# Kernel optimization log

Hardware: AMD Instinct MI355X
Metric: run time of the kernel (lower is better)

Reference implementation:

```python
import jax, jax.numpy as jnp
import numpy as np


def setup_inputs() -> dict:
    key = jax.random.key(0)
    k1, k2, k3 = jax.random.split(key, 3)
    B, L, H = 4, 4096, 1024
    x = jax.random.normal(k1, (B, L, H), dtype=jnp.float32)
    # 0.02 scale keeps attention logits in a sane range (like trained weights)
    in_proj_weight = jax.random.normal(k2, (3 * H, H), dtype=jnp.float32) * 0.02
    in_proj_bias = jnp.zeros((3 * H,), dtype=jnp.float32)
    out_proj_weight = jax.random.normal(k3, (H, H), dtype=jnp.float32) * 0.02
    out_proj_bias = jnp.zeros((H,), dtype=jnp.float32)
    return {
        "x": x,
        "in_proj_weight": in_proj_weight,
        "in_proj_bias": in_proj_bias,
        "out_proj_weight": out_proj_weight,
        "out_proj_bias": out_proj_bias,
        "num_heads": 16,
        "window_size": 128,
    }


def _windowed_mha(x, in_proj_weight, in_proj_bias, out_proj_weight, out_proj_bias,
                  num_heads, window_size):
    B, L, H = x.shape
    P = window_size
    pad = (-L) % P  # static
    xp = jnp.pad(x, ((0, 0), (0, pad), (0, 0))) if pad else x
    Lp = xp.shape[1]
    nw = Lp // P
    w = xp.reshape(B * nw, P, H)  # [NW, P, H]
    # packed QKV projection (torch MHA: q,k,v = split(x @ W_in.T + b_in))
    qkv = jnp.einsum('nph,dh->npd', w, in_proj_weight) + in_proj_bias
    q, k, v = jnp.split(qkv, 3, axis=-1)
    hd = H // num_heads

    def to_heads(t):
        return t.reshape(B * nw, P, num_heads, hd).transpose(0, 2, 1, 3)  # [NW, Hh, P, hd]

    q, k, v = to_heads(q), to_heads(k), to_heads(v)
    scale = 1.0 / jnp.sqrt(jnp.asarray(hd, dtype=x.dtype))
    scores = jnp.einsum('nhqd,nhkd->nhqk', q * scale, k)  # [NW, Hh, P, P]
    attn = jax.nn.softmax(scores, axis=-1)
    o = jnp.einsum('nhqk,nhkd->nhqd', attn, v)  # [NW, Hh, P, hd]
    o = o.transpose(0, 2, 1, 3).reshape(B * nw, P, H)
    o = jnp.einsum('nph,oh->npo', o, out_proj_weight) + out_proj_bias
    o = o.reshape(B, Lp, H)
    return o[:, :L]


def reference(x, in_proj_weight, in_proj_bias, out_proj_weight, out_proj_bias,
              num_heads, window_size):
    return _windowed_mha(x, in_proj_weight, in_proj_bias, out_proj_weight,
                         out_proj_bias, num_heads, window_size)
```

## Files before the change

### kernel.cpp

```cpp
#include <hip/hip_runtime.h>
#include <hip/hip_bf16.h>
#include <cstdint>


typedef __bf16 bf16_t;
typedef __bf16 bf16x8 __attribute__((ext_vector_type(8)));
typedef __bf16 bf16x4 __attribute__((ext_vector_type(4)));
typedef float  floatx4 __attribute__((ext_vector_type(4)));

#define MFMA_16x16x32(A, B, C) __builtin_amdgcn_mfma_f32_16x16x32_bf16(A, B, C, 0, 0, 0)

__device__ __forceinline__ void gld_lds16(const bf16_t* g, bf16_t* l) {
  __builtin_amdgcn_global_load_lds(
      (__attribute__((address_space(1))) void*)(void*)(g),
      (__attribute__((address_space(3))) void*)(l), 16, 0, 0);
}

__device__ __forceinline__ void cvt8(const float* __restrict__ s,
                                     bf16_t* __restrict__ d) {
  float4 a = ((const float4*)s)[0];
  float4 b = ((const float4*)s)[1];
  bf16x8 o;
  o[0] = (bf16_t)a.x; o[1] = (bf16_t)a.y; o[2] = (bf16_t)a.z; o[3] = (bf16_t)a.w;
  o[4] = (bf16_t)b.x; o[5] = (bf16_t)b.y; o[6] = (bf16_t)b.z; o[7] = (bf16_t)b.w;
  *(bf16x8*)d = o;
}

__global__ void cvt_all(const float* __restrict__ x,
                        const float* __restrict__ Win,
                        const float* __restrict__ Wout,
                        bf16_t* __restrict__ xb,
                        bf16_t* __restrict__ Wpk,
                        bf16_t* __restrict__ Woutb) {
  const int idx = blockIdx.x * 256 + threadIdx.x;
  if (idx < 2097152) {
    cvt8(x + (size_t)idx * 8, xb + (size_t)idx * 8);
  } else if (idx < 2228224) {
    const int i = idx - 2097152;
    cvt8(Wout + (size_t)i * 8, Woutb + (size_t)i * 8);
  } else {
    const int c = idx - 2228224;
    const int dr = c >> 7, i = c & 127;
    const int head = dr / 192, s = dr - head * 192;
    const int src = (s < 64) ? head * 64 + s
                  : (s < 128) ? 1024 + head * 64 + (s - 64)
                              : 2048 + head * 64 + (s - 128);
    cvt8(Win + (size_t)src * 1024 + i * 8, Wpk + (size_t)dr * 1024 + i * 8);
  }
}

__global__ __launch_bounds__(256, 2) void gemm_out(
    const bf16_t* __restrict__ A, const bf16_t* __restrict__ Bm,
    const float* __restrict__ bias, float* __restrict__ C,
    int M, int N, int K) {
  __shared__ bf16_t As[128 * 64];
  __shared__ bf16_t Bs[256 * 64];
  const int tid  = threadIdx.x;
  const int lane = tid & 63;
  const int wave = tid >> 6;
  const int n16  = lane & 15;
  const int q4   = lane >> 4;
  const int wm   = (wave >> 1) * 64;
  const int wn   = (wave & 1) * 128;
  const int m0   = blockIdx.y * 128;
  const int n0   = blockIdx.x * 256;

  floatx4 acc[4][8] = {};

  for (int k0 = 0; k0 < K; k0 += 64) {
    __syncthreads();
#pragma unroll
    for (int it = 0; it < 4; ++it) {
      const int ch = it * 256 + tid;
      const int r  = ch >> 3;
      const int c8 = (ch & 7) ^ (r & 7);
      gld_lds16(A + (size_t)(m0 + r) * K + k0 + c8 * 8,
                As + (it * 256 + wave * 64) * 8);
    }
#pragma unroll
    for (int it = 0; it < 8; ++it) {
      const int ch = it * 256 + tid;
      const int r  = ch >> 3;
      const int c8 = (ch & 7) ^ (r & 7);
      gld_lds16(Bm + (size_t)(n0 + r) * K + k0 + c8 * 8,
                Bs + (it * 256 + wave * 64) * 8);
    }
    __syncthreads();

#pragma unroll
    for (int half = 0; half < 2; ++half) {
      bf16x8 af[4], bfr[8];
#pragma unroll
      for (int i = 0; i < 4; ++i) {
        const int row = wm + i * 16 + n16;
        af[i] = *(const bf16x8*)&As[row * 64 + (((half * 4 + q4) ^ (row & 7)) * 8)];
      }
#pragma unroll
      for (int j = 0; j < 8; ++j) {
        const int row = wn + j * 16 + n16;
        bfr[j] = *(const bf16x8*)&Bs[row * 64 + (((half * 4 + q4) ^ (row & 7)) * 8)];
      }
#pragma unroll
      for (int i = 0; i < 4; ++i)
#pragma unroll
        for (int j = 0; j < 8; ++j)
          acc[i][j] = MFMA_16x16x32(af[i], bfr[j], acc[i][j]);
    }
  }

#pragma unroll
  for (int i = 0; i < 4; ++i)
#pragma unroll
    for (int j = 0; j < 8; ++j) {
      const int col = n0 + wn + j * 16 + n16;
      const float b = bias[col];
#pragma unroll
      for (int r = 0; r < 4; ++r) {
        const int row = m0 + wm + i * 16 + q4 * 4 + r;
        C[(size_t)row * N + col] = acc[i][j][r] + b;
      }
    }
}

__global__ __launch_bounds__(256, 3) void qkv_attn(
    const bf16_t* __restrict__ X,
    const bf16_t* __restrict__ Wpk,
    const float* __restrict__ bin,
    bf16_t* __restrict__ o)
{
  __shared__ bf16_t smem[26624];
  bf16_t* Xs  = smem;
  bf16_t* Ws  = smem + 8192;
  bf16_t* qs  = smem;
  bf16_t* ks  = smem + 9216;
  bf16_t* vsT = smem + 18432;
  bf16_t* Ps  = smem;

  const int wid  = blockIdx.x;
  const int h    = blockIdx.y;
  const int tid  = threadIdx.x;
  const int lane = tid & 63;
  const int wave = tid >> 6;
  const int n16  = lane & 15;
  const int q4   = lane >> 4;
  const int wm   = (wave >> 1) * 64;
  const int wn   = (wave & 1) * 96;

  const bf16_t* Xg = X + (size_t)wid * 128 * 1024;
  const bf16_t* Wg = Wpk + (size_t)h * 192 * 1024;

  floatx4 acc[4][6] = {};
  for (int k0 = 0; k0 < 1024; k0 += 64) {
    __syncthreads();
#pragma unroll
    for (int it = 0; it < 4; ++it) {
      const int ch = it * 256 + tid;
      const int r  = ch >> 3;
      const int c8 = (ch & 7) ^ (r & 7);
      gld_lds16(Xg + (size_t)r * 1024 + k0 + c8 * 8,
                Xs + (it * 256 + wave * 64) * 8);
    }
#pragma unroll
    for (int it = 0; it < 6; ++it) {
      const int ch = it * 256 + tid;
      const int r  = ch >> 3;
      const int c8 = (ch & 7) ^ (r & 7);
      gld_lds16(Wg + (size_t)r * 1024 + k0 + c8 * 8,
                Ws + (it * 256 + wave * 64) * 8);
    }
    __syncthreads();

#pragma unroll
    for (int half = 0; half < 2; ++half) {
      bf16x8 af[4], bfr[6];
#pragma unroll
      for (int i = 0; i < 4; ++i) {
        const int row = wm + i * 16 + n16;
        af[i] = *(const bf16x8*)&Xs[row * 64 + (((half * 4 + q4) ^ (row & 7)) * 8)];
      }
#pragma unroll
      for (int j = 0; j < 6; ++j) {
        const int row = wn + j * 16 + n16;
        bfr[j] = *(const bf16x8*)&Ws[row * 64 + (((half * 4 + q4) ^ (row & 7)) * 8)];
      }
#pragma unroll
      for (int i = 0; i < 4; ++i)
#pragma unroll
        for (int j = 0; j < 6; ++j)
          acc[i][j] = MFMA_16x16x32(af[i], bfr[j], acc[i][j]);
    }
  }
  __syncthreads();

#pragma unroll
  for (int j = 0; j < 6; ++j) {
    const int base = wn + j * 16;
    const int col  = base + n16;
    const int gb = (base < 64) ? h * 64 + col
                 : (base < 128) ? 1024 + h * 64 + (col - 64)
                                : 2048 + h * 64 + (col - 128);
    const float bias = bin[gb];
#pragma unroll
    for (int i = 0; i < 4; ++i) {
      const int row0 = wm + i * 16 + q4 * 4;
      if (base < 64) {
#pragma unroll
        for (int r = 0; r < 4; ++r)
          qs[(row0 + r) * 72 + col] = (bf16_t)((acc[i][j][r] + bias) * 0.125f);
      } else if (base < 128) {
#pragma unroll
        for (int r = 0; r < 4; ++r)
          ks[(row0 + r) * 72 + (col - 64)] = (bf16_t)(acc[i][j][r] + bias);
      } else {
        bf16x4 pv;
#pragma unroll
        for (int r = 0; r < 4; ++r) pv[r] = (bf16_t)(acc[i][j][r] + bias);
        const int d = col - 128;
        const int c8 = row0 >> 3, pos = row0 & 7;
        *(bf16x4*)&vsT[d * 128 + ((c8 ^ n16) << 3) + pos] = pv;
      }
    }
  }
  __syncthreads();

  floatx4 sacc[2][8] = {};
#pragma unroll
  for (int ks0 = 0; ks0 < 2; ++ks0) {
    bf16x8 aq[2];
#pragma unroll
    for (int i = 0; i < 2; ++i)
      aq[i] = *(const bf16x8*)&qs[(wave * 32 + i * 16 + n16) * 72 + ks0 * 32 + q4 * 8];
#pragma unroll
    for (int j = 0; j < 8; ++j) {
      bf16x8 bk = *(const bf16x8*)&ks[(j * 16 + n16) * 72 + ks0 * 32 + q4 * 8];
      sacc[0][j] = MFMA_16x16x32(aq[0], bk, sacc[0][j]);
      sacc[1][j] = MFMA_16x16x32(aq[1], bk, sacc[1][j]);
    }
  }
  __syncthreads();

  float invs[2][4];
#pragma unroll
  for (int i = 0; i < 2; ++i) {
#pragma unroll
    for (int r = 0; r < 4; ++r) {
      float vals[8];
      float s = 0.f;
#pragma unroll
      for (int j = 0; j < 8; ++j) {
        vals[j] = __expf(sacc[i][j][r]);
        s += vals[j];
      }
      for (int m = 1; m < 16; m <<= 1) s += __shfl_xor(s, m, 64);
      invs[i][r] = 1.0f / s;
      const int prow = wave * 32 + i * 16 + q4 * 4 + r;
#pragma unroll
      for (int j = 0; j < 8; ++j)
        Ps[prow * 136 + j * 16 + n16] = (bf16_t)vals[j];
    }
  }
  __syncthreads();

  floatx4 oacc[2][4] = {};
#pragma unroll
  for (int kk = 0; kk < 4; ++kk) {
    bf16x8 ap[2];
#pragma unroll
    for (int i = 0; i < 2; ++i)
      ap[i] = *(const bf16x8*)&Ps[(wave * 32 + i * 16 + n16) * 136 + kk * 32 + q4 * 8];
#pragma unroll
    for (int j = 0; j < 4; ++j) {
      const int d = j * 16 + n16;
      bf16x8 bv = *(const bf16x8*)&vsT[d * 128 + (((kk * 4 + q4) ^ n16) << 3)];
      oacc[0][j] = MFMA_16x16x32(ap[0], bv, oacc[0][j]);
      oacc[1][j] = MFMA_16x16x32(ap[1], bv, oacc[1][j]);
    }
  }

  bf16_t* go = o + (size_t)wid * 128 * 1024 + h * 64;
#pragma unroll
  for (int i = 0; i < 2; ++i)
#pragma unroll
    for (int j = 0; j < 4; ++j)
#pragma unroll
      for (int r = 0; r < 4; ++r) {
        const int row = wave * 32 + i * 16 + q4 * 4 + r;
        go[(size_t)row * 1024 + j * 16 + n16] = (bf16_t)(oacc[i][j][r] * invs[i][r]);
      }
}

extern "C" void kernel_launch(void* const* d_in, const int* in_sizes, int n_in,
                              void* d_out, int out_size, void* d_ws, size_t ws_size,
                              hipStream_t stream) {
  const float* x    = (const float*)d_in[0];
  const float* Win  = (const float*)d_in[1];
  const float* bin  = (const float*)d_in[2];
  const float* Wout = (const float*)d_in[3];
  const float* bout = (const float*)d_in[4];
  float* out = (float*)d_out;

  const size_t M = 16384, H = 1024, H3 = 3072;

  bf16_t* xb    = (bf16_t*)d_ws;
  bf16_t* Wpk   = xb + M * H;
  bf16_t* Woutb = Wpk + H3 * H;
  bf16_t* ob    = Woutb + H * H;

  cvt_all<<<dim3(10240), 256, 0, stream>>>(x, Win, Wout, xb, Wpk, Woutb);

  qkv_attn<<<dim3(128, 16), 256, 0, stream>>>(xb, Wpk, bin, ob);

  gemm_out<<<dim3((unsigned)(H / 256), (unsigned)(M / 128)), 256, 0, stream>>>(
      ob, Woutb, bout, out, (int)M, (int)H, (int)H);
}
```

Baseline: 285.5 us.

## Double-buffer LDS tiles with K=32 stages in QKV and out-proj GEMMs

Both GEMM main loops now use two LDS buffers with a K-step of 32 instead of one buffer with K-step 64. Global-to-LDS loads for stage t+2 are issued while stage t is computed, using explicit vmcnt waits and raw barriers in place of __syncthreads. The MFMA block runs at raised wave priority via s_setprio. This targets exposed global-load latency, at the cost of twice as many barriers per K and hard-coded wait counts that assume K=1024.

```diff
diff --git a/kernel.cpp b/kernel.cpp
--- a/kernel.cpp
+++ b/kernel.cpp
@@ -53,8 +53,7 @@
     const bf16_t* __restrict__ A, const bf16_t* __restrict__ Bm,
     const float* __restrict__ bias, float* __restrict__ C,
     int M, int N, int K) {
-  __shared__ bf16_t As[128 * 64];
-  __shared__ bf16_t Bs[256 * 64];
+  __shared__ __align__(16) bf16_t smem[2][128 * 32 + 256 * 32];
   const int tid  = threadIdx.x;
   const int lane = tid & 63;
   const int wave = tid >> 6;
@@ -67,46 +66,66 @@
 
   floatx4 acc[4][8] = {};
 
-  for (int k0 = 0; k0 < K; k0 += 64) {
-    __syncthreads();
-#pragma unroll
-    for (int it = 0; it < 4; ++it) {
-      const int ch = it * 256 + tid;
-      const int r  = ch >> 3;
-      const int c8 = (ch & 7) ^ (r & 7);
-      gld_lds16(A + (size_t)(m0 + r) * K + k0 + c8 * 8,
-                As + (it * 256 + wave * 64) * 8);
-    }
-#pragma unroll
-    for (int it = 0; it < 8; ++it) {
-      const int ch = it * 256 + tid;
-      const int r  = ch >> 3;
-      const int c8 = (ch & 7) ^ (r & 7);
-      gld_lds16(Bm + (size_t)(n0 + r) * K + k0 + c8 * 8,
-                Bs + (it * 256 + wave * 64) * 8);
-    }
-    __syncthreads();
-
-#pragma unroll
-    for (int half = 0; half < 2; ++half) {
-      bf16x8 af[4], bfr[8];
-#pragma unroll
-      for (int i = 0; i < 4; ++i) {
-        const int row = wm + i * 16 + n16;
-        af[i] = *(const bf16x8*)&As[row * 64 + (((half * 4 + q4) ^ (row & 7)) * 8)];
-      }
-#pragma unroll
-      for (int j = 0; j < 8; ++j) {
-        const int row = wn + j * 16 + n16;
-        bfr[j] = *(const bf16x8*)&Bs[row * 64 + (((half * 4 + q4) ^ (row & 7)) * 8)];
-      }
-#pragma unroll
-      for (int i = 0; i < 4; ++i)
-#pragma unroll
-        for (int j = 0; j < 8; ++j)
-          acc[i][j] = MFMA_16x16x32(af[i], bfr[j], acc[i][j]);
-    }
-  }
+#define GO_STAGE(BUF, K0)                                                   \
+  {                                                                         \
+    bf16_t* Ad = smem[BUF];                                                 \
+    bf16_t* Bd = smem[BUF] + 128 * 32;                                      \
+    _Pragma("unroll")                                                       \
+    for (int it = 0; it < 2; ++it) {                \
+      const int ch = it * 256 + tid;                                        \
+      const int r  = ch >> 2, c8 = (ch & 3) ^ (r & 3);                      \
+      gld_lds16(A + (size_t)(m0 + r) * K + (K0) + c8 * 8,                   \
+                Ad + (it * 256 + wave * 64) * 8);                           \
+    }                                                                       \
+    _Pragma("unroll")                                                       \
+    for (int it = 0; it < 4; ++it) {               \
+      const int ch = it * 256 + tid;                                        \
+      const int r  = ch >> 2, c8 = (ch & 3) ^ (r & 3);                      \
+      gld_lds16(Bm + (size_t)(n0 + r) * K + (K0) + c8 * 8,                  \
+                Bd + (it * 256 + wave * 64) * 8);                           \
+    }                                                                       \
+  }
+
+#define GO_ITER(T, BUF)                                                     \
+  {                                                                         \
+    if ((T) < 31) { asm volatile("s_waitcnt vmcnt(6)" ::: "memory"); }      \
+    else          { asm volatile("s_waitcnt vmcnt(0)" ::: "memory"); }      \
+    __builtin_amdgcn_s_barrier();                                           \
+    __builtin_amdgcn_sched_barrier(0);                                      \
+    const bf16_t* As_ = smem[BUF];                                          \
+    const bf16_t* Bs_ = smem[BUF] + 128 * 32;                               \
+    bf16x8 af[4], bfr[8];                                                   \
+    _Pragma("unroll")                                                       \
+    for (int i = 0; i < 4; ++i) {                                           \
+      const int row = wm + i * 16 + n16;                                    \
+      af[i] = *(const bf16x8*)&As_[row * 32 + ((q4 ^ (row & 3)) * 8)];      \
+    }                                                                       \
+    _Pragma("unroll")                                                       \
+    for (int j = 0; j < 8; ++j) {                                           \
+      const int row = wn + j * 16 + n16;                                    \
+      bfr[j] = *(const bf16x8*)&Bs_[row * 32 + ((q4 ^ (row & 3)) * 8)];     \
+    }                                                                       \
+    __builtin_amdgcn_s_setprio(1);                                          \
+    _Pragma("unroll")                                                       \
+    for (int i = 0; i < 4; ++i)                                             \
+      _Pragma("unroll")                                                     \
+      for (int j = 0; j < 8; ++j)                                           \
+        acc[i][j] = MFMA_16x16x32(af[i], bfr[j], acc[i][j]);                \
+    __builtin_amdgcn_s_setprio(0);                                          \
+    asm volatile("s_waitcnt lgkmcnt(0)" ::: "memory");                      \
+    __builtin_amdgcn_s_barrier();                                           \
+    __builtin_amdgcn_sched_barrier(0);                                      \
+    if ((T) + 2 < 32) GO_STAGE(BUF, ((T) + 2) * 32)                         \
+  }
+
+  GO_STAGE(0, 0)
+  GO_STAGE(1, 32)
+  for (int t = 0; t < 32; t += 2) {
+    GO_ITER(t, 0)
+    GO_ITER(t + 1, 1)
+  }
+#undef GO_ITER
+#undef GO_STAGE
 
 #pragma unroll
   for (int i = 0; i < 4; ++i)
@@ -128,9 +147,7 @@
     const float* __restrict__ bin,
     bf16_t* __restrict__ o)
 {
-  __shared__ bf16_t smem[26624];
-  bf16_t* Xs  = smem;
-  bf16_t* Ws  = smem + 8192;
+  __shared__ __align__(16) bf16_t smem[26624];
   bf16_t* qs  = smem;
   bf16_t* ks  = smem + 9216;
   bf16_t* vsT = smem + 18432;
@@ -150,47 +167,67 @@
   const bf16_t* Wg = Wpk + (size_t)h * 192 * 1024;
 
   floatx4 acc[4][6] = {};
-  for (int k0 = 0; k0 < 1024; k0 += 64) {
-    __syncthreads();
-#pragma unroll
-    for (int it = 0; it < 4; ++it) {
-      const int ch = it * 256 + tid;
-      const int r  = ch >> 3;
-      const int c8 = (ch & 7) ^ (r & 7);
-      gld_lds16(Xg + (size_t)r * 1024 + k0 + c8 * 8,
-                Xs + (it * 256 + wave * 64) * 8);
-    }
-#pragma unroll
-    for (int it = 0; it < 6; ++it) {
-      const int ch = it * 256 + tid;
-      const int r  = ch >> 3;
-      const int c8 = (ch & 7) ^ (r & 7);
-      gld_lds16(Wg + (size_t)r * 1024 + k0 + c8 * 8,
-                Ws + (it * 256 + wave * 64) * 8);
-    }
-    __syncthreads();
-
-#pragma unroll
-    for (int half = 0; half < 2; ++half) {
-      bf16x8 af[4], bfr[6];
-#pragma unroll
-      for (int i = 0; i < 4; ++i) {
-        const int row = wm + i * 16 + n16;
-        af[i] = *(const bf16x8*)&Xs[row * 64 + (((half * 4 + q4) ^ (row & 7)) * 8)];
-      }
-#pragma unroll
-      for (int j = 0; j < 6; ++j) {
-        const int row = wn + j * 16 + n16;
-        bfr[j] = *(const bf16x8*)&Ws[row * 64 + (((half * 4 + q4) ^ (row & 7)) * 8)];
-      }
-#pragma unroll
-      for (int i = 0; i < 4; ++i)
-#pragma unroll
-        for (int j = 0; j < 6; ++j)
-          acc[i][j] = MFMA_16x16x32(af[i], bfr[j], acc[i][j]);
-    }
-  }
-  __syncthreads();
+
+#define QKV_STAGE(BUF, K0)                                                  \
+  {                                                                         \
+    bf16_t* Xd = smem + (BUF) * 10240;                                      \
+    bf16_t* Wd = Xd + 4096;                                                 \
+    _Pragma("unroll")                                                       \
+    for (int it = 0; it < 2; ++it) {                \
+      const int ch = it * 256 + tid;                                        \
+      const int r  = ch >> 2, c8 = (ch & 3) ^ (r & 3);                      \
+      gld_lds16(Xg + (size_t)r * 1024 + (K0) + c8 * 8,                      \
+                Xd + (it * 256 + wave * 64) * 8);                           \
+    }                                                                       \
+    _Pragma("unroll")                                                       \
+    for (int it = 0; it < 3; ++it) {                \
+      const int ch = it * 256 + tid;                                        \
+      const int r  = ch >> 2, c8 = (ch & 3) ^ (r & 3);                      \
+      gld_lds16(Wg + (size_t)r * 1024 + (K0) + c8 * 8,                      \
+                Wd + (it * 256 + wave * 64) * 8);                           \
+    }                                                                       \
+  }
+
+#define QKV_ITER(T, BUF)                                                    \
+  {                                                                         \
+    if ((T) < 31) { asm volatile("s_waitcnt vmcnt(5)" ::: "memory"); }      \
+    else          { asm volatile("s_waitcnt vmcnt(0)" ::: "memory"); }      \
+    __builtin_amdgcn_s_barrier();                                           \
+    __builtin_amdgcn_sched_barrier(0);                                      \
+    const bf16_t* Xb = smem + (BUF) * 10240;                                \
+    const bf16_t* Wb = Xb + 4096;                                           \
+    bf16x8 af[4], bfr[6];                                                   \
+    _Pragma("unroll")                                                       \
+    for (int i = 0; i < 4; ++i) {                                           \
+      const int row = wm + i * 16 + n16;                                    \
+      af[i] = *(const bf16x8*)&Xb[row * 32 + ((q4 ^ (row & 3)) * 8)];       \
+    }                                                                       \
+    _Pragma("unroll")                                                       \
+    for (int j = 0; j < 6; ++j) {                                           \
+      const int row = wn + j * 16 + n16;                                    \
+      bfr[j] = *(const bf16x8*)&Wb[row * 32 + ((q4 ^ (row & 3)) * 8)];      \
+    }                                                                       \
+    __builtin_amdgcn_s_setprio(1);                                          \
+    _Pragma("unroll")                                                       \
+    for (int i = 0; i < 4; ++i)                                             \
+      _Pragma("unroll")                                                     \
+      for (int j = 0; j < 6; ++j)                                           \
+        acc[i][j] = MFMA_16x16x32(af[i], bfr[j], acc[i][j]);                \
+    __builtin_amdgcn_s_setprio(0);                                          \
+    asm volatile("s_waitcnt lgkmcnt(0)" ::: "memory");                      \
+    __builtin_amdgcn_s_barrier();                                           \
+    __builtin_amdgcn_sched_barrier(0);                                      \
+    if ((T) + 2 < 32) QKV_STAGE(BUF, ((T) + 2) * 32)                        \
+  }
+
+  QKV_STAGE(0, 0)
+  QKV_STAGE(1, 32)
+  for (int t = 0; t < 32; t += 2) {
+    QKV_ITER(t, 0)
+    QKV_ITER(t + 1, 1)
+  }
+#undef QKV_ITER
+#undef QKV_STAGE
 
 #pragma unroll
   for (int j = 0; j < 6; ++j) {
```

Result: slower. 296.0 us (+3.7%).
